# Optimization experiments

Measured on AMD Instinct MI355X. Metric: run time of the kernel, lower is better.

Reference implementation:

```python
import jax, jax.numpy as jnp
import numpy as np
import math

B, S, D, H = 8, 256, 4096, 16
HD = D // H  # 256 == S, so the module's transposed mask application is exactly elementwise


def setup_inputs() -> dict:
    key = jax.random.key(0)
    ks = jax.random.split(key, 12)
    sc = 1.0 / math.sqrt(D)
    inp = {
        "q": jax.random.normal(ks[0], (B, S, D), dtype=jnp.float32),
        "k": jax.random.normal(ks[1], (B, S, D), dtype=jnp.float32),
        "v": jax.random.normal(ks[2], (B, S, D), dtype=jnp.float32),
        "mask": jax.random.randint(ks[3], (B, S), 0, 2),
        "Wq": jax.random.normal(ks[4], (D, D), dtype=jnp.float32) * sc,
        "bq": jnp.zeros((D,), dtype=jnp.float32),
        "Wk": jax.random.normal(ks[5], (D, D), dtype=jnp.float32) * sc,
        "bk": jnp.zeros((D,), dtype=jnp.float32),
        "Wv": jax.random.normal(ks[6], (D, D), dtype=jnp.float32) * sc,
        "bv": jnp.zeros((D,), dtype=jnp.float32),
        "Wo": jax.random.normal(ks[7], (D, D), dtype=jnp.float32) * sc,
        "bo": jnp.zeros((D,), dtype=jnp.float32),
    }
    return inp


def reference(q, k, v, mask, Wq, bq, Wk, bk, Wv, bv, Wo, bo):
    def proj(x, W, b):
        # nn.Linear: x @ W.T + b ; then [B,S,H,HD] -> [B,H,S,HD]
        return (x @ W.T + b).reshape(B, S, H, HD).transpose(0, 2, 1, 3)

    qh = proj(q, Wq, bq)
    kh = proj(k, Wk, bk)
    vh = proj(v, Wv, bv)

    # torch: attn_mask = (mask==0).view(bs,1,1,-1).repeat(1,H,HD,1) -> [B,H,HD,S]
    # then where(attn_mask, 0, q) against q of shape [B,H,S,HD] (elementwise since HD==S)
    am = jnp.broadcast_to((mask == 0)[:, None, None, :], (B, H, HD, S))
    qh = jnp.where(am, 0.0, qh)
    kh = jnp.where(am, 0.0, kh)

    scale = 1.0 / math.sqrt(HD)
    scores = jnp.einsum('bhqd,bhkd->bhqk', qh, kh) * scale
    w = jax.nn.softmax(scores, axis=-1)
    out = jnp.einsum('bhqk,bhkd->bhqd', w, vh)
    out = out.transpose(0, 2, 1, 3).reshape(B, S, D)
    out = out * (D ** -0.5)
    return out @ Wo.T + bo
```

## Files before the change

kernel.cpp:

```cpp
#include <hip/hip_runtime.h>


typedef _Float16 f16;
typedef f16 f16x8 __attribute__((ext_vector_type(8)));
typedef float f32x4 __attribute__((ext_vector_type(4)));

__device__ __forceinline__ void g2lds(const f16* g, f16* l) {
  __builtin_amdgcn_global_load_lds((const __attribute__((address_space(1))) void*)g,
                                   (__attribute__((address_space(3))) void*)l, 16, 0, 0);
}

__global__ __launch_bounds__(256) void cvt_kernel(const float* __restrict__ in,
                                                  f16* __restrict__ out, int n) {
  int i = (blockIdx.x * 256 + threadIdx.x) * 8;
  if (i >= n) return;
  float4 a = *(const float4*)(in + i);
  float4 b = *(const float4*)(in + i + 4);
  f16x8 o;
  o[0] = (f16)a.x; o[1] = (f16)a.y; o[2] = (f16)a.z; o[3] = (f16)a.w;
  o[4] = (f16)b.x; o[5] = (f16)b.y; o[6] = (f16)b.z; o[7] = (f16)b.w;
  *(f16x8*)(out + i) = o;
}

template<int EPI>
__global__ __launch_bounds__(512, 2) void gemm_dp(
    const f16* __restrict__ A, const f16* __restrict__ B,
    const float* __restrict__ bias, const int* __restrict__ mask,
    void* __restrict__ out, int M, int N, int K)
{
  __shared__ __align__(16) f16 lds[3 * 24576];
  const int tid = threadIdx.x;
  const int lane = tid & 63, wid = tid >> 6;
  const int wm = wid >> 2, wn = wid & 3;
  const int ln = lane & 15, lh = lane >> 4;
  const int bm = blockIdx.y, bn = blockIdx.x;

  const size_t Abase = (size_t)bm * 128 * K;
  const size_t Bbase = (size_t)bn * 256 * K;

  const int sr = tid >> 3;
  const int ss = (tid & 7) ^ (sr & 7);

  const int NT = K >> 6;

#define STAGE(t, part)                                                          \
  do {                                                                          \
    const int kt_ = (t) << 6;                                                   \
    f16* bo_ = &lds[((t) % 3) * 24576];                                         \
    if ((part) == 0) {                                                          \
      g2lds(A + Abase + (size_t)sr * K + kt_ + ss * 8,         bo_ + tid * 8);  \
      g2lds(B + Bbase + (size_t)sr * K + kt_ + ss * 8,         bo_ + 8192 + tid * 8); \
      g2lds(B + Bbase + (size_t)(64 + sr) * K + kt_ + ss * 8,  bo_ + 8192 + (512 + tid) * 8); \
    } else {                                                                    \
      g2lds(A + Abase + (size_t)(64 + sr) * K + kt_ + ss * 8,  bo_ + (512 + tid) * 8); \
      g2lds(B + Bbase + (size_t)(128 + sr) * K + kt_ + ss * 8, bo_ + 8192 + (1024 + tid) * 8); \
      g2lds(B + Bbase + (size_t)(192 + sr) * K + kt_ + ss * 8, bo_ + 8192 + (1536 + tid) * 8); \
    }                                                                           \
  } while (0)

  f32x4 acc[4][4] = {};

  STAGE(0, 0); STAGE(0, 1);
  STAGE(1, 0); STAGE(1, 1);
  asm volatile("s_waitcnt vmcnt(6)" ::: "memory");
  __builtin_amdgcn_s_barrier();

  const int sl0 = lh;
  const int sl1 = 4 + lh;
  const int lx = ln & 7;

  for (int t = 0; t < NT; ++t) {
    const f16* bA = &lds[(t % 3) * 24576];
    const f16* bB = bA + 8192;

    f16x8 a0[4], b0[4];
#pragma unroll
    for (int mf = 0; mf < 4; ++mf)
      a0[mf] = *(const f16x8*)&bA[(wm * 64 + mf * 16 + ln) * 64 + (sl0 ^ lx) * 8];
#pragma unroll
    for (int nf = 0; nf < 4; ++nf)
      b0[nf] = *(const f16x8*)&bB[(wn * 64 + nf * 16 + ln) * 64 + (sl0 ^ lx) * 8];
    if (t + 2 < NT) STAGE(t + 2, 0);
    asm volatile("" ::: "memory");
    __builtin_amdgcn_s_barrier();
    __builtin_amdgcn_s_setprio(1);
#pragma unroll
    for (int mf = 0; mf < 4; ++mf)
#pragma unroll
      for (int nf = 0; nf < 4; ++nf)
        acc[mf][nf] = __builtin_amdgcn_mfma_f32_16x16x32_f16(a0[mf], b0[nf], acc[mf][nf], 0, 0, 0);
    __builtin_amdgcn_s_setprio(0);
    asm volatile("" ::: "memory");
    __builtin_amdgcn_s_barrier();

    f16x8 a1[4], b1[4];
#pragma unroll
    for (int mf = 0; mf < 4; ++mf)
      a1[mf] = *(const f16x8*)&bA[(wm * 64 + mf * 16 + ln) * 64 + (sl1 ^ lx) * 8];
#pragma unroll
    for (int nf = 0; nf < 4; ++nf)
      b1[nf] = *(const f16x8*)&bB[(wn * 64 + nf * 16 + ln) * 64 + (sl1 ^ lx) * 8];
    if (t + 2 < NT) STAGE(t + 2, 1);
    asm volatile("" ::: "memory");
    __builtin_amdgcn_s_barrier();
    __builtin_amdgcn_s_setprio(1);
#pragma unroll
    for (int mf = 0; mf < 4; ++mf)
#pragma unroll
      for (int nf = 0; nf < 4; ++nf)
        acc[mf][nf] = __builtin_amdgcn_mfma_f32_16x16x32_f16(a1[mf], b1[nf], acc[mf][nf], 0, 0, 0);
    __builtin_amdgcn_s_setprio(0);
    if (t + 2 < NT) {
      asm volatile("s_waitcnt vmcnt(6)" ::: "memory");
    } else if (t + 1 < NT) {
      asm volatile("s_waitcnt vmcnt(0)" ::: "memory");
    }
    asm volatile("" ::: "memory");
    __builtin_amdgcn_s_barrier();
  }
#undef STAGE

#pragma unroll
  for (int mf = 0; mf < 4; ++mf)
#pragma unroll
    for (int nf = 0; nf < 4; ++nf)
#pragma unroll
      for (int i = 0; i < 4; ++i) {
        int R = bm * 128 + wm * 64 + mf * 16 + lh * 4 + i;
        int C = bn * 256 + wn * 64 + nf * 16 + ln;
        float v = acc[mf][nf][i];
        if (EPI == 0) {
          v += bias[C];
          v = mask[(R >> 8) * 256 + (C & 255)] ? v : 0.0f;
          ((f16*)out)[(size_t)((R >> 8) * 16 + (C >> 8)) * 65536 +
                      (size_t)(R & 255) * 256 + (C & 255)] = (f16)v;
        } else if (EPI == 1) {
          v += bias[R];
          ((f16*)out)[(size_t)(C >> 8) * 1048576 + (size_t)R * 256 + (C & 255)] = (f16)v;
        } else {
          v += bias[C];
          ((float*)out)[(size_t)R * N + C] = v;
        }
      }
}

__global__ __launch_bounds__(256) void attn_kernel(
    const f16* __restrict__ Q, const f16* __restrict__ Kt,
    const f16* __restrict__ Vt, f16* __restrict__ aout)
{
  __shared__ __align__(16) f16 tile[64 * 256];
  __shared__ __align__(16) f16 pbuf[64 * 256];
  const int tid = threadIdx.x;
  const int lane = tid & 63, w = tid >> 6;
  const int ln = lane & 15, lh = lane >> 4;
  const int bh = blockIdx.x >> 2, rb = blockIdx.x & 3;
  const int b = bh >> 4, h = bh & 15;
  const size_t hb = (size_t)bh * 65536;

  const int strow = tid >> 5;
  const int stsl  = (tid & 31) ^ (strow & 7);

  f16x8 aq[8];
  {
    const f16* qp = Q + hb + (size_t)(rb * 64 + w * 16 + ln) * 256;
#pragma unroll
    for (int ks = 0; ks < 8; ++ks)
      aq[ks] = *(const f16x8*)(qp + ks * 32 + lh * 8);
  }

  f32x4 sacc[16] = {};

  for (int kt = 0; kt < 4; ++kt) {
#pragma unroll
    for (int c = 0; c < 8; ++c) {
      int L = c * 256 + tid;
      int row = c * 8 + strow;
      g2lds(Kt + hb + (size_t)(kt * 64 + row) * 256 + stsl * 8, &tile[L * 8]);
    }
    __syncthreads();
#pragma unroll
    for (int nf = 0; nf < 4; ++nf) {
      f16x8 bf[8];
#pragma unroll
      for (int ks = 0; ks < 8; ++ks) {
        int r = nf * 16 + ln;
        int sl = (ks * 4 + lh) ^ (r & 7);
        bf[ks] = *(const f16x8*)&tile[r * 256 + sl * 8];
      }
#pragma unroll
      for (int ks = 0; ks < 8; ++ks)
        sacc[kt * 4 + nf] = __builtin_amdgcn_mfma_f32_16x16x32_f16(
            aq[ks], bf[ks], sacc[kt * 4 + nf], 0, 0, 0);
    }
    __syncthreads();
  }

  const float SC = 1.0f / 16.0f;
  float mrow[4] = {-1e30f, -1e30f, -1e30f, -1e30f};
#pragma unroll
  for (int t = 0; t < 16; ++t)
#pragma unroll
    for (int i = 0; i < 4; ++i) mrow[i] = fmaxf(mrow[i], sacc[t][i]);
#pragma unroll
  for (int i = 0; i < 4; ++i) {
    mrow[i] = fmaxf(mrow[i], __shfl_xor(mrow[i], 1));
    mrow[i] = fmaxf(mrow[i], __shfl_xor(mrow[i], 2));
    mrow[i] = fmaxf(mrow[i], __shfl_xor(mrow[i], 4));
    mrow[i] = fmaxf(mrow[i], __shfl_xor(mrow[i], 8));
  }
  float ssum[4] = {0.f, 0.f, 0.f, 0.f};
#pragma unroll
  for (int t = 0; t < 16; ++t)
#pragma unroll
    for (int i = 0; i < 4; ++i) {
      float p = __expf((sacc[t][i] - mrow[i]) * SC);
      sacc[t][i] = p;
      ssum[i] += p;
    }
#pragma unroll
  for (int i = 0; i < 4; ++i) {
    ssum[i] += __shfl_xor(ssum[i], 1);
    ssum[i] += __shfl_xor(ssum[i], 2);
    ssum[i] += __shfl_xor(ssum[i], 4);
    ssum[i] += __shfl_xor(ssum[i], 8);
  }
  float rs[4];
#pragma unroll
  for (int i = 0; i < 4; ++i) rs[i] = 1.0f / ssum[i];

#pragma unroll
  for (int t = 0; t < 16; ++t)
#pragma unroll
    for (int i = 0; i < 4; ++i) {
      int row = w * 16 + lh * 4 + i;
      int col = (t >> 2) * 64 + (t & 3) * 16 + ln;
      pbuf[row * 256 + (col ^ ((row & 7) << 3))] = (f16)(sacc[t][i] * rs[i]);
    }

  f16x8 pa[8];
  {
    int r = w * 16 + ln;
#pragma unroll
    for (int ks = 0; ks < 8; ++ks) {
      int col = ks * 32 + lh * 8;
      pa[ks] = *(const f16x8*)&pbuf[r * 256 + (col ^ ((r & 7) << 3))];
    }
  }

  for (int dt = 0; dt < 4; ++dt) {
#pragma unroll
    for (int c = 0; c < 8; ++c) {
      int L = c * 256 + tid;
      int row = c * 8 + strow;
      g2lds(Vt + hb + (size_t)(dt * 64 + row) * 256 + stsl * 8, &tile[L * 8]);
    }
    __syncthreads();
    f32x4 oacc[4] = {};
#pragma unroll
    for (int nf = 0; nf < 4; ++nf) {
      f16x8 bf[8];
#pragma unroll
      for (int ks = 0; ks < 8; ++ks) {
        int r = nf * 16 + ln;
        int sl = (ks * 4 + lh) ^ (r & 7);
        bf[ks] = *(const f16x8*)&tile[r * 256 + sl * 8];
      }
#pragma unroll
      for (int ks = 0; ks < 8; ++ks)
        oacc[nf] = __builtin_amdgcn_mfma_f32_16x16x32_f16(pa[ks], bf[ks], oacc[nf], 0, 0, 0);
    }
#pragma unroll
    for (int nf = 0; nf < 4; ++nf)
#pragma unroll
      for (int i = 0; i < 4; ++i) {
        int s = rb * 64 + w * 16 + lh * 4 + i;
        int d = dt * 64 + nf * 16 + ln;
        aout[(size_t)(b * 256 + s) * 4096 + h * 256 + d] = (f16)(oacc[nf][i] * 0.015625f);
      }
    __syncthreads();
  }
}

extern "C" void kernel_launch(void* const* d_in, const int* in_sizes, int n_in,
                              void* d_out, int out_size, void* d_ws, size_t ws_size,
                              hipStream_t stream) {
  const float* q  = (const float*)d_in[0];
  const float* k  = (const float*)d_in[1];
  const float* v  = (const float*)d_in[2];
  const int*   mk = (const int*)d_in[3];
  const float* Wq = (const float*)d_in[4];
  const float* bq = (const float*)d_in[5];
  const float* Wk = (const float*)d_in[6];
  const float* bk = (const float*)d_in[7];
  const float* Wv = (const float*)d_in[8];
  const float* bv = (const float*)d_in[9];
  const float* Wo = (const float*)d_in[10];
  const float* bo = (const float*)d_in[11];
  float* out = (float*)d_out;

  const size_t NQ = 2048ull * 4096;
  const size_t NW = 4096ull * 4096;
  f16* ws = (f16*)d_ws;
  f16* q16  = ws;
  f16* k16  = q16 + NQ;
  f16* v16  = k16 + NQ;
  f16* Wq16 = v16 + NQ;
  f16* Wk16 = Wq16 + NW;
  f16* Wv16 = Wk16 + NW;
  f16* Wo16 = Wv16 + NW;
  f16* Qbh  = Wo16 + NW;
  f16* Kbh  = Qbh + NQ;
  f16* Vt   = Kbh + NQ;
  f16* at16 = Vt + NQ;

  cvt_kernel<<<(int)(NQ / 2048), 256, 0, stream>>>(q, q16, (int)NQ);
  cvt_kernel<<<(int)(NQ / 2048), 256, 0, stream>>>(k, k16, (int)NQ);
  cvt_kernel<<<(int)(NQ / 2048), 256, 0, stream>>>(v, v16, (int)NQ);
  cvt_kernel<<<(int)(NW / 2048), 256, 0, stream>>>(Wq, Wq16, (int)NW);
  cvt_kernel<<<(int)(NW / 2048), 256, 0, stream>>>(Wk, Wk16, (int)NW);
  cvt_kernel<<<(int)(NW / 2048), 256, 0, stream>>>(Wv, Wv16, (int)NW);
  cvt_kernel<<<(int)(NW / 2048), 256, 0, stream>>>(Wo, Wo16, (int)NW);

  gemm_dp<0><<<dim3(16, 16), 512, 0, stream>>>(q16, Wq16, bq, mk, Qbh, 2048, 4096, 4096);
  gemm_dp<0><<<dim3(16, 16), 512, 0, stream>>>(k16, Wk16, bk, mk, Kbh, 2048, 4096, 4096);
  gemm_dp<1><<<dim3(8, 32), 512, 0, stream>>>(Wv16, v16, bv, nullptr, Vt, 4096, 2048, 4096);
  attn_kernel<<<512, 256, 0, stream>>>(Qbh, Kbh, Vt, at16);
  gemm_dp<2><<<dim3(16, 16), 512, 0, stream>>>(at16, Wo16, bo, nullptr, out, 2048, 4096, 4096);
}
```

Baseline: 410.2 us.

## Software-pipeline LDS fragment loads with MFMA and cut barriers per K-tile

Restructures the GEMM main loop so the LDS fragment loads for the next half-tile are issued before the MFMAs of the current half-tile, with register double-buffering (ca/cb, na/nb). Both global-to-LDS stage halves are issued together, and the rotating pointers replace the modulo buffer indexing. Barriers per K-tile drop from four to two. The aim is to hide LDS read latency behind MFMA work and reduce synchronisation, at the cost of more live registers, which could lower occupancy or cause spills.

```diff
diff --git a/kernel.cpp b/kernel.cpp
--- a/kernel.cpp
+++ b/kernel.cpp
@@ -43,82 +43,89 @@
 
   const int NT = K >> 6;
 
-#define STAGE(t, part)                                                          \
+  f16* p0 = &lds[0];
+  f16* p1 = &lds[24576];
+  f16* p2 = &lds[2 * 24576];
+
+#define STAGE(t_, bo_, part)                                                    \
   do {                                                                          \
-    const int kt_ = (t) << 6;                                                   \
-    f16* bo_ = &lds[((t) % 3) * 24576];                                         \
+    const int kt_ = (t_) << 6;                                                  \
     if ((part) == 0) {                                                          \
-      g2lds(A + Abase + (size_t)sr * K + kt_ + ss * 8,         bo_ + tid * 8);  \
-      g2lds(B + Bbase + (size_t)sr * K + kt_ + ss * 8,         bo_ + 8192 + tid * 8); \
-      g2lds(B + Bbase + (size_t)(64 + sr) * K + kt_ + ss * 8,  bo_ + 8192 + (512 + tid) * 8); \
+      g2lds(A + Abase + (size_t)sr * K + kt_ + ss * 8,         (bo_) + tid * 8);  \
+      g2lds(B + Bbase + (size_t)sr * K + kt_ + ss * 8,         (bo_) + 8192 + tid * 8); \
+      g2lds(B + Bbase + (size_t)(64 + sr) * K + kt_ + ss * 8,  (bo_) + 8192 + (512 + tid) * 8); \
     } else {                                                                    \
-      g2lds(A + Abase + (size_t)(64 + sr) * K + kt_ + ss * 8,  bo_ + (512 + tid) * 8); \
-      g2lds(B + Bbase + (size_t)(128 + sr) * K + kt_ + ss * 8, bo_ + 8192 + (1024 + tid) * 8); \
-      g2lds(B + Bbase + (size_t)(192 + sr) * K + kt_ + ss * 8, bo_ + 8192 + (1536 + tid) * 8); \
+      g2lds(A + Abase + (size_t)(64 + sr) * K + kt_ + ss * 8,  (bo_) + (512 + tid) * 8); \
+      g2lds(B + Bbase + (size_t)(128 + sr) * K + kt_ + ss * 8, (bo_) + 8192 + (1024 + tid) * 8); \
+      g2lds(B + Bbase + (size_t)(192 + sr) * K + kt_ + ss * 8, (bo_) + 8192 + (1536 + tid) * 8); \
     }                                                                           \
   } while (0)
 
+  const int lx = ln & 7;
+  const int arow = (wm * 64 + ln) * 64;
+  const int brow = (wn * 64 + ln) * 64;
+
+#define LOADFRAGS(fa, fb, buf, ks)                                              \
+  do {                                                                          \
+    const f16* bA_ = (buf);                                                     \
+    const f16* bB_ = (buf) + 8192;                                              \
+    const int so_ = (((ks) * 4 + lh) ^ lx) * 8;                                 \
+    _Pragma("unroll")                                                           \
+    for (int mf = 0; mf < 4; ++mf)                                              \
+      fa[mf] = *(const f16x8*)&bA_[arow + mf * 1024 + so_];                     \
+    _Pragma("unroll")                                                           \
+    for (int nf = 0; nf < 4; ++nf)                                              \
+      fb[nf] = *(const f16x8*)&bB_[brow + nf * 1024 + so_];                     \
+  } while (0)
+
+#define MFMA16(fa, fb)                                                          \
+  do {                                                                          \
+    __builtin_amdgcn_s_setprio(1);                                              \
+    _Pragma("unroll")                                                           \
+    for (int mf = 0; mf < 4; ++mf)                                              \
+      _Pragma("unroll")                                                         \
+      for (int nf = 0; nf < 4; ++nf)                                            \
+        acc[mf][nf] = __builtin_amdgcn_mfma_f32_16x16x32_f16(fa[mf], fb[nf],    \
+                                                             acc[mf][nf], 0, 0, 0); \
+    __builtin_amdgcn_s_setprio(0);                                              \
+  } while (0)
+
   f32x4 acc[4][4] = {};
-
-  STAGE(0, 0); STAGE(0, 1);
-  STAGE(1, 0); STAGE(1, 1);
+  f16x8 ca[4], cb[4], na[4], nb[4];
+
+  STAGE(0, p0, 0); STAGE(0, p0, 1);
+  STAGE(1, p1, 0); STAGE(1, p1, 1);
   asm volatile("s_waitcnt vmcnt(6)" ::: "memory");
   __builtin_amdgcn_s_barrier();
-
-  const int sl0 = lh;
-  const int sl1 = 4 + lh;
-  const int lx = ln & 7;
+  asm volatile("" ::: "memory");
+  LOADFRAGS(ca, cb, p0, 0);
 
   for (int t = 0; t < NT; ++t) {
-    const f16* bA = &lds[(t % 3) * 24576];
-    const f16* bB = bA + 8192;
-
-    f16x8 a0[4], b0[4];
-#pragma unroll
-    for (int mf = 0; mf < 4; ++mf)
-      a0[mf] = *(const f16x8*)&bA[(wm * 64 + mf * 16 + ln) * 64 + (sl0 ^ lx) * 8];
-#pragma unroll
-    for (int nf = 0; nf < 4; ++nf)
-      b0[nf] = *(const f16x8*)&bB[(wn * 64 + nf * 16 + ln) * 64 + (sl0 ^ lx) * 8];
-    if (t + 2 < NT) STAGE(t + 2, 0);
-    asm volatile("" ::: "memory");
-    __builtin_amdgcn_s_barrier();
-    __builtin_amdgcn_s_setprio(1);
-#pragma unroll
-    for (int mf = 0; mf < 4; ++mf)
-#pragma unroll
-      for (int nf = 0; nf < 4; ++nf)
-        acc[mf][nf] = __builtin_amdgcn_mfma_f32_16x16x32_f16(a0[mf], b0[nf], acc[mf][nf], 0, 0, 0);
-    __builtin_amdgcn_s_setprio(0);
-    asm volatile("" ::: "memory");
-    __builtin_amdgcn_s_barrier();
-
-    f16x8 a1[4], b1[4];
-#pragma unroll
-    for (int mf = 0; mf < 4; ++mf)
-      a1[mf] = *(const f16x8*)&bA[(wm * 64 + mf * 16 + ln) * 64 + (sl1 ^ lx) * 8];
-#pragma unroll
-    for (int nf = 0; nf < 4; ++nf)
-      b1[nf] = *(const f16x8*)&bB[(wn * 64 + nf * 16 + ln) * 64 + (sl1 ^ lx) * 8];
-    if (t + 2 < NT) STAGE(t + 2, 1);
-    asm volatile("" ::: "memory");
-    __builtin_amdgcn_s_barrier();
-    __builtin_amdgcn_s_setprio(1);
-#pragma unroll
-    for (int mf = 0; mf < 4; ++mf)
-#pragma unroll
-      for (int nf = 0; nf < 4; ++nf)
-        acc[mf][nf] = __builtin_amdgcn_mfma_f32_16x16x32_f16(a1[mf], b1[nf], acc[mf][nf], 0, 0, 0);
-    __builtin_amdgcn_s_setprio(0);
-    if (t + 2 < NT) {
-      asm volatile("s_waitcnt vmcnt(6)" ::: "memory");
-    } else if (t + 1 < NT) {
-      asm volatile("s_waitcnt vmcnt(0)" ::: "memory");
-    }
-    asm volatile("" ::: "memory");
-    __builtin_amdgcn_s_barrier();
+    LOADFRAGS(na, nb, p0, 1);
+    if (t + 2 < NT) { STAGE(t + 2, p2, 0); STAGE(t + 2, p2, 1); }
+    MFMA16(ca, cb);
+
+    if (t + 1 < NT) {
+      if (t + 2 < NT) {
+        asm volatile("s_waitcnt vmcnt(6)" ::: "memory");
+      } else {
+        asm volatile("s_waitcnt vmcnt(0)" ::: "memory");
+      }
+      __builtin_amdgcn_s_barrier();
+      asm volatile("" ::: "memory");
+      LOADFRAGS(ca, cb, p1, 0);
+      MFMA16(na, nb);
+      asm volatile("" ::: "memory");
+      __builtin_amdgcn_s_barrier();
+      asm volatile("" ::: "memory");
+      f16* tp = p0; p0 = p1; p1 = p2; p2 = tp;
+    } else {
+      MFMA16(na, nb);
+    }
   }
 #undef STAGE
+#undef LOADFRAGS
+#undef MFMA16
 
 #pragma unroll
   for (int mf = 0; mf < 4; ++mf)
```

Measured after the change: 403.0 us. About the same (-1.8%).
